# Optimization experiments

Measured on AMD Instinct MI355X. Metric: run time of the kernel, lower is better.

## Reference

```python
import jax, jax.numpy as jnp
import numpy as np

SCALE = 1.0

def setup_inputs() -> dict:
    key = jax.random.key(0)
    k1, k2 = jax.random.split(key)
    feats = jax.random.normal(k1, (8, 512, 128, 128), dtype=jnp.float32)
    probs = jax.random.normal(k2, (8, 19, 128, 128), dtype=jnp.float32)
    return {"feats": feats, "probs": probs}

def reference(feats, probs):
    B, K, H, W = probs.shape
    C = feats.shape[1]
    p = probs.reshape(B, K, H * W)            # (B, K, HW)
    f = feats.reshape(B, C, H * W)            # (B, C, HW)
    attn = jax.nn.softmax(SCALE * p, axis=2)  # softmax over spatial dim
    # (B, K, HW) @ (B, HW, C) -> (B, K, C)
    ctx = jnp.einsum('bkn,bcn->bkc', attn, f)
    # permute to (B, C, K) and add trailing singleton dim -> (B, C, K, 1)
    return jnp.transpose(ctx, (0, 2, 1))[..., None]
```

## Files before the change

kernel.cpp:

```cpp
#include <hip/hip_runtime.h>
#include <hip/hip_bf16.h>
#include <math.h>

#define BATCH 8
#define KK 19
#define CC 512
#define HW 16384
#define HW4 (HW/4)

__global__ __launch_bounds__(256) void softmax_rows(const float* __restrict__ probs,
                                                    float* __restrict__ attn) {
    const int row = blockIdx.x;
    const float4* p = (const float4*)(probs + (size_t)row * HW);
    float4* a = (float4*)(attn + (size_t)row * HW);
    const int t = threadIdx.x;

    float4 v[16];
    float m = -INFINITY;
#pragma unroll
    for (int i = 0; i < 16; ++i) {
        v[i] = p[i * 256 + t];
        m = fmaxf(m, fmaxf(fmaxf(v[i].x, v[i].y), fmaxf(v[i].z, v[i].w)));
    }
#pragma unroll
    for (int off = 32; off; off >>= 1) m = fmaxf(m, __shfl_xor(m, off));

    __shared__ float redmax[4];
    __shared__ float redsum[4];
    if ((t & 63) == 0) redmax[t >> 6] = m;
    __syncthreads();
    const float rowmax = fmaxf(fmaxf(redmax[0], redmax[1]), fmaxf(redmax[2], redmax[3]));

    float s = 0.f;
#pragma unroll
    for (int i = 0; i < 16; ++i) {
        v[i].x = __expf(v[i].x - rowmax);
        v[i].y = __expf(v[i].y - rowmax);
        v[i].z = __expf(v[i].z - rowmax);
        v[i].w = __expf(v[i].w - rowmax);
        s += (v[i].x + v[i].y) + (v[i].z + v[i].w);
    }
#pragma unroll
    for (int off = 32; off; off >>= 1) s += __shfl_xor(s, off);
    if ((t & 63) == 0) redsum[t >> 6] = s;
    __syncthreads();
    const float rs = 1.0f / (redsum[0] + redsum[1] + redsum[2] + redsum[3]);

#pragma unroll
    for (int i = 0; i < 16; ++i) {
        float4 o;
        o.x = v[i].x * rs; o.y = v[i].y * rs; o.z = v[i].z * rs; o.w = v[i].w * rs;
        a[i * 256 + t] = o;
    }
}

__global__ __launch_bounds__(256, 4) void ctx_kernel(const float* __restrict__ feats,
                                                     const float* __restrict__ attn,
                                                     float* __restrict__ out) {
    const int cblk = blockIdx.x;
    const int b    = blockIdx.y;
    const int t    = threadIdx.x;
    const int wave = t >> 6;
    const int lane = t & 63;
    const int c0 = cblk * 4;

    const float4* f = (const float4*)(feats + ((size_t)b * CC + c0) * HW);
    const float4* a = (const float4*)(attn + (size_t)b * KK * HW);

    float acc[KK][4];
#pragma unroll
    for (int k = 0; k < KK; ++k)
#pragma unroll
        for (int ci = 0; ci < 4; ++ci) acc[k][ci] = 0.f;

    const int nq0 = wave * (HW4 / 4) + lane;

#pragma unroll 1
    for (int it = 0; it < 16; ++it) {
        const int nq = nq0 + it * 64;
        float4 fv[4];
#pragma unroll
        for (int ci = 0; ci < 4; ++ci) fv[ci] = f[(size_t)ci * HW4 + nq];
#pragma unroll
        for (int k = 0; k < KK; ++k) {
            const float4 av = a[(size_t)k * HW4 + nq];
#pragma unroll
            for (int ci = 0; ci < 4; ++ci) {
                acc[k][ci] += av.x * fv[ci].x + av.y * fv[ci].y
                            + av.z * fv[ci].z + av.w * fv[ci].w;
            }
        }
    }

#pragma unroll
    for (int k = 0; k < KK; ++k) {
#pragma unroll
        for (int ci = 0; ci < 4; ++ci) {
            float s = acc[k][ci];
#pragma unroll
            for (int off = 32; off; off >>= 1) s += __shfl_xor(s, off);
            acc[k][ci] = s;
        }
    }

    __shared__ float part[4][KK * 4];
    if (lane == 0) {
#pragma unroll
        for (int k = 0; k < KK; ++k)
#pragma unroll
            for (int ci = 0; ci < 4; ++ci)
                part[wave][k * 4 + ci] = acc[k][ci];
    }
    __syncthreads();

    if (t < KK * 4) {
        const float s = part[0][t] + part[1][t] + part[2][t] + part[3][t];
        const int k = t >> 2;
        const int ci = t & 3;
        out[((size_t)b * CC + (c0 + ci)) * KK + k] = s;
    }
}

extern "C" void kernel_launch(void* const* d_in, const int* in_sizes, int n_in,
                              void* d_out, int out_size, void* d_ws, size_t ws_size,
                              hipStream_t stream) {
    const float* feats = (const float*)d_in[0];
    const float* probs = (const float*)d_in[1];
    float* out = (float*)d_out;
    float* attn = (float*)d_ws;

    softmax_rows<<<BATCH * KK, 256, 0, stream>>>(probs, attn);
    ctx_kernel<<<dim3(CC / 4, BATCH), 256, 0, stream>>>(feats, attn, out);
}
```

Baseline: 441.8 us.

## Share attention tiles across waves via LDS double buffering and split HW with atomics

The context kernel now gives each wave its own 4 channels, so the four waves of a block share one attention tile. That tile is staged into LDS with global_load_lds and double-buffered. The spatial dimension is split four ways across blocks, and partial sums are merged with atomicAdd into an output zeroed by a new kernel. Softmax switches to an online max/sum pass followed by a reload pass, which lowers register pressure but reads probs twice. The intent is to cut redundant global reads of attention per channel, at the cost of atomics, an extra launch and a per-iteration barrier.

```diff
diff --git a/kernel.cpp b/kernel.cpp
--- a/kernel.cpp
+++ b/kernel.cpp
@@ -7,6 +7,12 @@
 #define CC 512
 #define HW 16384
 #define HW4 (HW/4)
+#define NSPLIT 4
+#define ITERS (HW4/(NSPLIT*64))
+
+__global__ __launch_bounds__(256) void zero_out(float4* __restrict__ out) {
+    out[blockIdx.x * 256 + threadIdx.x] = make_float4(0.f, 0.f, 0.f, 0.f);
+}
 
 __global__ __launch_bounds__(256) void softmax_rows(const float* __restrict__ probs,
                                                     float* __restrict__ attn) {
@@ -15,57 +21,80 @@
     float4* a = (float4*)(attn + (size_t)row * HW);
     const int t = threadIdx.x;
 
-    float4 v[16];
-    float m = -INFINITY;
-#pragma unroll
+    float m = -INFINITY, s = 0.f;
+#pragma unroll 4
     for (int i = 0; i < 16; ++i) {
-        v[i] = p[i * 256 + t];
-        m = fmaxf(m, fmaxf(fmaxf(v[i].x, v[i].y), fmaxf(v[i].z, v[i].w)));
+        float4 v = p[i * 256 + t];
+        float mx = fmaxf(fmaxf(v.x, v.y), fmaxf(v.z, v.w));
+        float mn = fmaxf(m, mx);
+        s = s * __expf(m - mn)
+          + __expf(v.x - mn) + __expf(v.y - mn) + __expf(v.z - mn) + __expf(v.w - mn);
+        m = mn;
     }
 #pragma unroll
-    for (int off = 32; off; off >>= 1) m = fmaxf(m, __shfl_xor(m, off));
+    for (int off = 32; off; off >>= 1) {
+        float mo = __shfl_xor(m, off);
+        float so = __shfl_xor(s, off);
+        float mn = fmaxf(m, mo);
+        s = s * __expf(m - mn) + so * __expf(mo - mn);
+        m = mn;
+    }
+    __shared__ float sm[4], ss[4];
+    if ((t & 63) == 0) { sm[t >> 6] = m; ss[t >> 6] = s; }
+    __syncthreads();
+    const float M = fmaxf(fmaxf(sm[0], sm[1]), fmaxf(sm[2], sm[3]));
+    const float S = ss[0] * __expf(sm[0] - M) + ss[1] * __expf(sm[1] - M)
+                  + ss[2] * __expf(sm[2] - M) + ss[3] * __expf(sm[3] - M);
+    const float inv = 1.0f / S;
 
-    __shared__ float redmax[4];
-    __shared__ float redsum[4];
-    if ((t & 63) == 0) redmax[t >> 6] = m;
-    __syncthreads();
-    const float rowmax = fmaxf(fmaxf(redmax[0], redmax[1]), fmaxf(redmax[2], redmax[3]));
-
-    float s = 0.f;
-#pragma unroll
+#pragma unroll 4
     for (int i = 0; i < 16; ++i) {
-        v[i].x = __expf(v[i].x - rowmax);
-        v[i].y = __expf(v[i].y - rowmax);
-        v[i].z = __expf(v[i].z - rowmax);
-        v[i].w = __expf(v[i].w - rowmax);
-        s += (v[i].x + v[i].y) + (v[i].z + v[i].w);
-    }
-#pragma unroll
-    for (int off = 32; off; off >>= 1) s += __shfl_xor(s, off);
-    if ((t & 63) == 0) redsum[t >> 6] = s;
-    __syncthreads();
-    const float rs = 1.0f / (redsum[0] + redsum[1] + redsum[2] + redsum[3]);
-
-#pragma unroll
-    for (int i = 0; i < 16; ++i) {
+        float4 v = p[i * 256 + t];
         float4 o;
-        o.x = v[i].x * rs; o.y = v[i].y * rs; o.z = v[i].z * rs; o.w = v[i].w * rs;
+        o.x = __expf(v.x - M) * inv;
+        o.y = __expf(v.y - M) * inv;
+        o.z = __expf(v.z - M) * inv;
+        o.w = __expf(v.w - M) * inv;
         a[i * 256 + t] = o;
     }
 }
 
-__global__ __launch_bounds__(256, 4) void ctx_kernel(const float* __restrict__ feats,
-                                                     const float* __restrict__ attn,
-                                                     float* __restrict__ out) {
+__global__ __launch_bounds__(256) __attribute__((amdgpu_waves_per_eu(4, 4)))
+void ctx_kernel(const float* __restrict__ feats,
+                const float* __restrict__ attn,
+                float* __restrict__ out) {
     const int cblk = blockIdx.x;
     const int b    = blockIdx.y;
+    const int ns   = blockIdx.z;
     const int t    = threadIdx.x;
     const int wave = t >> 6;
     const int lane = t & 63;
-    const int c0 = cblk * 4;
+    const int c0   = cblk * 16 + wave * 4;
 
-    const float4* f = (const float4*)(feats + ((size_t)b * CC + c0) * HW);
-    const float4* a = (const float4*)(attn + (size_t)b * KK * HW);
+    __shared__ float4 abuf[2][KK][64];
+
+    const float4* af = (const float4*)attn  + (size_t)b * KK * HW4;
+    const float4* ff = (const float4*)feats + ((size_t)b * CC + c0) * HW4;
+
+    const int nbase0 = ns * ITERS * 64;
+
+    #define STAGE(buf, nb)                                                      \
+        do {                                                                    \
+            _Pragma("unroll")                                                   \
+            for (int j = 0; j < 5; ++j) {                                       \
+                const int row = j * 4 + wave;                                   \
+                if (row < KK) {                                                 \
+                    const float4* src = af + (size_t)row * HW4 + (nb) + lane;   \
+                    __builtin_amdgcn_global_load_lds(                           \
+                        (const __attribute__((address_space(1))) void*)src,     \
+                        (__attribute__((address_space(3))) void*)&abuf[buf][row][0], \
+                        16, 0, 0);                                              \
+                }                                                               \
+            }                                                                   \
+        } while (0)
+
+    STAGE(0, nbase0);
+    __syncthreads();
 
     float acc[KK][4];
 #pragma unroll
@@ -73,24 +102,30 @@
 #pragma unroll
         for (int ci = 0; ci < 4; ++ci) acc[k][ci] = 0.f;
 
-    const int nq0 = wave * (HW4 / 4) + lane;
-
+    int cur = 0;
 #pragma unroll 1
-    for (int it = 0; it < 16; ++it) {
-        const int nq = nq0 + it * 64;
+    for (int it = 0; it < ITERS; ++it) {
+        if (it + 1 < ITERS) {
+            if (cur == 0) STAGE(1, nbase0 + (it + 1) * 64);
+            else          STAGE(0, nbase0 + (it + 1) * 64);
+        }
+        const int nq = nbase0 + it * 64 + lane;
         float4 fv[4];
 #pragma unroll
-        for (int ci = 0; ci < 4; ++ci) fv[ci] = f[(size_t)ci * HW4 + nq];
+        for (int ci = 0; ci < 4; ++ci) fv[ci] = ff[(size_t)ci * HW4 + nq];
 #pragma unroll
         for (int k = 0; k < KK; ++k) {
-            const float4 av = a[(size_t)k * HW4 + nq];
+            const float4 av = abuf[cur][k][lane];
 #pragma unroll
             for (int ci = 0; ci < 4; ++ci) {
                 acc[k][ci] += av.x * fv[ci].x + av.y * fv[ci].y
                             + av.z * fv[ci].z + av.w * fv[ci].w;
             }
         }
+        __syncthreads();
+        cur ^= 1;
     }
+    #undef STAGE
 
 #pragma unroll
     for (int k = 0; k < KK; ++k) {
@@ -103,21 +138,12 @@
         }
     }
 
-    __shared__ float part[4][KK * 4];
     if (lane == 0) {
 #pragma unroll
         for (int k = 0; k < KK; ++k)
 #pragma unroll
             for (int ci = 0; ci < 4; ++ci)
-                part[wave][k * 4 + ci] = acc[k][ci];
-    }
-    __syncthreads();
-
-    if (t < KK * 4) {
-        const float s = part[0][t] + part[1][t] + part[2][t] + part[3][t];
-        const int k = t >> 2;
-        const int ci = t & 3;
-        out[((size_t)b * CC + (c0 + ci)) * KK + k] = s;
+                atomicAdd(&out[((size_t)b * CC + (c0 + ci)) * KK + k], acc[k][ci]);
     }
 }
 
@@ -129,6 +155,7 @@
     float* out = (float*)d_out;
     float* attn = (float*)d_ws;
 
+    zero_out<<<(CC * KK * BATCH) / (256 * 4), 256, 0, stream>>>((float4*)out);
     softmax_rows<<<BATCH * KK, 256, 0, stream>>>(probs, attn);
-    ctx_kernel<<<dim3(CC / 4, BATCH), 256, 0, stream>>>(feats, attn, out);
+    ctx_kernel<<<dim3(CC / 16, BATCH, NSPLIT), 256, 0, stream>>>(feats, attn, out);
 }
```

After: 583.7 us. 1.32x slower.
